# Optimization experiments

Measured on AMD Instinct MI355X. Metric: run time of the kernel, lower is better.

## Reference

```python
import jax, jax.numpy as jnp
import numpy as np

HIDDEN = 1024
HEADS = 16
HEAD_DIM = HIDDEN // HEADS


def setup_inputs() -> dict:
    key = jax.random.key(0)
    ks = jax.random.split(key, 8)
    B, S = 2, 2048
    scale = 1.0 / np.sqrt(HIDDEN)
    inp = {
        "hidden_states": jax.random.normal(ks[0], (B, S, HIDDEN), dtype=jnp.float32),
        "attention_mask": jnp.zeros((B, 1, 1, S), dtype=jnp.float32),
        "q_w": jax.random.normal(ks[1], (HIDDEN, HIDDEN), dtype=jnp.float32) * scale,
        "q_b": jnp.zeros((HIDDEN,), dtype=jnp.float32),
        "k_w": jax.random.normal(ks[2], (HIDDEN, HIDDEN), dtype=jnp.float32) * scale,
        "k_b": jnp.zeros((HIDDEN,), dtype=jnp.float32),
        "v_w": jax.random.normal(ks[3], (HIDDEN, HIDDEN), dtype=jnp.float32) * scale,
        "v_b": jnp.zeros((HIDDEN,), dtype=jnp.float32),
    }
    return inp


def _split_heads(x):
    # [B, S, H] -> [B, heads, S, head_dim]
    B, S, _ = x.shape
    return x.reshape(B, S, HEADS, HEAD_DIM).transpose(0, 2, 1, 3)


def reference(hidden_states, attention_mask, q_w, q_b, k_w, k_b, v_w, v_b):
    # Linear projections (torch Linear: x @ W.T + b; here weights stored as [in, out])
    q = _split_heads(hidden_states @ q_w + q_b)  # [B, h, S, d]
    k = _split_heads(hidden_states @ k_w + k_b)
    v = _split_heads(hidden_states @ v_w + v_b)

    scores = jnp.einsum("bhqd,bhkd->bhqk", q, k) / jnp.sqrt(jnp.float32(HEAD_DIM))
    scores = scores + attention_mask  # additive mask, broadcast [B,1,1,S]
    probs = jax.nn.softmax(scores, axis=-1)
    # dropout prob = 0.0 -> identity
    ctx = jnp.einsum("bhqk,bhkd->bhqd", probs, v)  # [B, h, S, d]
    B, _, S, _ = ctx.shape
    ctx = ctx.transpose(0, 2, 1, 3).reshape(B, S, HIDDEN)
    return ctx
```

## Files before the change

### kernel.cpp

```cpp
#include <hip/hip_runtime.h>

typedef __bf16 bf16;
typedef __attribute__((ext_vector_type(8))) __bf16 bf16x8;
typedef __attribute__((ext_vector_type(4))) __bf16 bf16x4;
typedef __attribute__((ext_vector_type(4))) float f32x4;
typedef __attribute__((ext_vector_type(2))) unsigned int uint2v;
typedef __attribute__((ext_vector_type(4))) unsigned int uint4v;

#define MFMA(a, b, c) __builtin_amdgcn_mfma_f32_16x16x32_bf16((a), (b), (c), 0, 0, 0)
#define LOG2E 1.44269504088896340736f

__device__ __forceinline__ bf16x8 cvt8(float4 a, float4 b) {
  bf16x8 r;
  r[0] = (bf16)a.x; r[1] = (bf16)a.y; r[2] = (bf16)a.z; r[3] = (bf16)a.w;
  r[4] = (bf16)b.x; r[5] = (bf16)b.y; r[6] = (bf16)b.z; r[7] = (bf16)b.w;
  return r;
}

__device__ __forceinline__ void stage16(const bf16* g, bf16* l) {
  __builtin_amdgcn_global_load_lds(
      (const __attribute__((address_space(1))) void*)g,
      (__attribute__((address_space(3))) void*)l, 16, 0, 0);
}

__global__ __launch_bounds__(256)
void cvt(const float* __restrict__ hs, const float* __restrict__ qw,
         const float* __restrict__ kw, const float* __restrict__ vw,
         bf16* __restrict__ Xb, bf16* __restrict__ Wt) {
  const int bid = blockIdx.x, tid = threadIdx.x;
  if (bid < 2048) {
    size_t off = (size_t)bid * 2048 + tid * 8;
    float4 x0 = *(const float4*)(hs + off);
    float4 x1 = *(const float4*)(hs + off + 4);
    *(bf16x8*)(Xb + off) = cvt8(x0, x1);
  } else {
    int t = bid - 2048;
    int z = t >> 8, ti = t & 255;
    const float* W = (z == 0) ? qw : (z == 1) ? kw : vw;
    int k0 = (ti >> 4) * 64, n0 = (ti & 15) * 64;
    __shared__ bf16 T[64 * 72];
    #pragma unroll
    for (int i = 0; i < 16; ++i) {
      int e = i * 256 + tid;
      int kr = e >> 6, nc = e & 63;
      T[nc * 72 + kr] = (bf16)W[(size_t)(k0 + kr) * 1024 + n0 + nc];
    }
    __syncthreads();
    #pragma unroll
    for (int i = 0; i < 2; ++i) {
      int e = i * 256 + tid;
      int nr = e >> 3, kg = e & 7;
      *(bf16x8*)(Wt + (size_t)z * 1048576 + (size_t)(n0 + nr) * 1024 + k0 + kg * 8) =
          *(const bf16x8*)&T[nr * 72 + kg * 8];
    }
  }
}

__global__ __launch_bounds__(256, 3)
void qkv_gemm(const bf16* __restrict__ Xb, const bf16* __restrict__ Wt,
              const float* __restrict__ qbias, const float* __restrict__ kbias,
              const float* __restrict__ vbias,
              bf16* __restrict__ qo, bf16* __restrict__ ko, bf16* __restrict__ vo) {
  const int blk = blockIdx.x;
  const int xcd = blk & 7, slot = blk >> 3;
  const int mb = xcd * 4 + slot / 24;
  const int nb = slot % 24;
  const int z = nb >> 3, nbm = nb & 7;
  const bf16* W = Wt + (size_t)z * 1048576;

  const int tid = threadIdx.x;
  const int wave = tid >> 6, lane = tid & 63, quad = lane >> 4, c = lane & 15;
  const int wr = wave >> 1, wc = wave & 1;
  const int lrow = lane >> 3;
  const int lg = (lane & 7) ^ lrow;

  __shared__ bf16 As[128 * 64];
  __shared__ bf16 Bs[128 * 64];

  f32x4 acc[4][4] = {};

  for (int k0 = 0; k0 < 1024; k0 += 64) {
    #pragma unroll
    for (int i = 0; i < 4; ++i) {
      int r = wave * 32 + i * 8;
      stage16(Xb + (size_t)(mb * 128 + r + lrow) * 1024 + k0 + lg * 8, &As[r * 64]);
      stage16(W + (size_t)(nbm * 128 + r + lrow) * 1024 + k0 + lg * 8, &Bs[r * 64]);
    }
    __syncthreads();
    #pragma unroll
    for (int ch = 0; ch < 2; ++ch) {
      bf16x8 af[4];
      #pragma unroll
      for (int rt = 0; rt < 4; ++rt) {
        int row = wr * 64 + rt * 16 + c;
        af[rt] = *(const bf16x8*)&As[row * 64 + ((((ch << 2) | quad) ^ (c & 7)) << 3)];
      }
      #pragma unroll
      for (int nt = 0; nt < 4; ++nt) {
        int row = wc * 64 + nt * 16 + c;
        bf16x8 bfrag = *(const bf16x8*)&Bs[row * 64 + ((((ch << 2) | quad) ^ (c & 7)) << 3)];
        #pragma unroll
        for (int rt = 0; rt < 4; ++rt)
          acc[rt][nt] = MFMA(af[rt], bfrag, acc[rt][nt]);
      }
    }
    __syncthreads();
  }

  const float* bias = (z == 0) ? qbias : (z == 1) ? kbias : vbias;
  float bv[4];
  #pragma unroll
  for (int nt = 0; nt < 4; ++nt)
    bv[nt] = bias[nbm * 128 + wc * 64 + nt * 16 + c];

  if (z == 2) {
    #pragma unroll
    for (int rt = 0; rt < 4; ++rt)
      #pragma unroll
      for (int nt = 0; nt < 4; ++nt) {
        int m0 = mb * 128 + wr * 64 + rt * 16 + 4 * quad;
        int n = nbm * 128 + wc * 64 + nt * 16 + c;
        bf16x4 pk;
        #pragma unroll
        for (int reg = 0; reg < 4; ++reg) pk[reg] = (bf16)(acc[rt][nt][reg] + bv[nt]);
        int b = m0 >> 11, s0 = m0 & 2047, h = n >> 6, d = n & 63;
        *(bf16x4*)&vo[(((size_t)b * 16 + h) * 64 + d) * 2048 + s0] = pk;
      }
  } else {
    bf16* dst = (z == 0) ? qo : ko;
    const float scale = (z == 0) ? 0.125f * LOG2E : 1.0f;
    #pragma unroll
    for (int rt = 0; rt < 4; ++rt)
      #pragma unroll
      for (int nt = 0; nt < 4; ++nt)
        #pragma unroll
        for (int reg = 0; reg < 4; ++reg) {
          float v = (acc[rt][nt][reg] + bv[nt]) * scale;
          int m = mb * 128 + wr * 64 + rt * 16 + 4 * quad + reg;
          int n = nbm * 128 + wc * 64 + nt * 16 + c;
          int b = m >> 11, s = m & 2047, h = n >> 6, d = n & 63;
          dst[(((size_t)b * 16 + h) * 2048 + s) * 64 + d] = (bf16)v;
        }
  }
}

__global__ __launch_bounds__(256, 4)
void attn(const bf16* __restrict__ qg, const bf16* __restrict__ kg,
          const bf16* __restrict__ vtg, const float* __restrict__ mask,
          float* __restrict__ out) {
  const int blk = blockIdx.x;
  const int xcd = blk & 7, slot = blk >> 3;
  const int bh = xcd * 4 + (slot >> 5);
  const int qblk = slot & 31;
  const int b = bh >> 4, h = bh & 15;
  const int tid = threadIdx.x;
  const int wave = tid >> 6, lane = tid & 63, quad = lane >> 4, c = lane & 15;
  const int lrow = lane >> 3, lg = (lane & 7) ^ lrow;

  __shared__ __align__(16) bf16 Ks[2][64 * 64];
  __shared__ __align__(16) bf16 Vs[2][64 * 64];
  __shared__ __align__(16) float Ms[2048];

  const bf16* qb_ = qg + (size_t)bh * 2048 * 64;
  const bf16* kb_ = kg + (size_t)bh * 2048 * 64;
  const bf16* vb_ = vtg + (size_t)bh * 64 * 2048;

  #pragma unroll
  for (int i = 0; i < 2; ++i) {
    int idx = i * 1024 + tid * 4;
    float4 m = *(const float4*)&mask[b * 2048 + idx];
    float4 ms = {m.x * LOG2E, m.y * LOG2E, m.z * LOG2E, m.w * LOG2E};
    *(float4*)&Ms[idx] = ms;
  }

  bf16x8 qf[2];
  #pragma unroll
  for (int ch = 0; ch < 2; ++ch)
    qf[ch] = *(const bf16x8*)(qb_ +
        (size_t)(qblk * 64 + wave * 16 + c) * 64 + ch * 32 + quad * 8);

  #pragma unroll
  for (int i = 0; i < 2; ++i) {
    int r = wave * 16 + i * 8;
    stage16(kb_ + (size_t)(r + lrow) * 64 + lg * 8, &Ks[0][r * 64]);
    stage16(vb_ + (size_t)(r + lrow) * 2048 + lg * 8, &Vs[0][r * 64]);
  }
  __asm__ volatile("s_waitcnt lgkmcnt(0)" ::: "memory");

  f32x4 o[4] = {};
  float lsum2[2] = {0.f, 0.f};

  for (int kt = 0; kt < 32; ++kt) {
    const int cur = kt & 1;
    __asm__ volatile("s_waitcnt vmcnt(0)" ::: "memory");
    __builtin_amdgcn_s_barrier();
    __builtin_amdgcn_sched_barrier(0);

    if (kt < 31) {
      #pragma unroll
      for (int i = 0; i < 2; ++i) {
        int r = wave * 16 + i * 8;
        stage16(kb_ + (size_t)((kt + 1) * 64 + r + lrow) * 64 + lg * 8,
                &Ks[cur ^ 1][r * 64]);
        stage16(vb_ + (size_t)(r + lrow) * 2048 + (kt + 1) * 64 + lg * 8,
                &Vs[cur ^ 1][r * 64]);
      }
    }
    __builtin_amdgcn_sched_barrier(0);

    f32x4 s[4];
    #pragma unroll
    for (int nt = 0; nt < 4; ++nt) {
      float4 mv = *(const float4*)&Ms[kt * 64 + nt * 16 + 4 * quad];
      f32x4 sv = {mv.x, mv.y, mv.z, mv.w};
      s[nt] = sv;
    }

    __builtin_amdgcn_s_setprio(1);
    #pragma unroll
    for (int nt = 0; nt < 4; ++nt)
      #pragma unroll
      for (int ch = 0; ch < 2; ++ch) {
        bf16x8 kf = *(const bf16x8*)&Ks[cur][(nt * 16 + c) * 64 +
                                            ((((ch << 2) | quad) ^ (c & 7)) << 3)];
        s[nt] = MFMA(kf, qf[ch], s[nt]);
      }
    __builtin_amdgcn_s_setprio(0);

    unsigned int U[4][2];
    #pragma unroll
    for (int nt = 0; nt < 4; ++nt) {
      bf16x4 pk;
      #pragma unroll
      for (int reg = 0; reg < 4; ++reg) {
        float p = __builtin_amdgcn_exp2f(s[nt][reg]);
        lsum2[nt & 1] += p;
        pk[reg] = (bf16)p;
      }
      uint2v uu = __builtin_bit_cast(uint2v, pk);
      U[nt][0] = uu.x; U[nt][1] = uu.y;
    }
    bf16x8 pa[2];
    #pragma unroll
    for (int ch = 0; ch < 2; ++ch) {
      unsigned int X0 = U[2 * ch][0],     X1 = U[2 * ch][1];
      unsigned int Y0 = U[2 * ch + 1][0], Y1 = U[2 * ch + 1][1];
      __asm__ volatile("v_permlane32_swap_b32 %0, %1" : "+v"(X0), "+v"(Y0));
      __asm__ volatile("v_permlane32_swap_b32 %0, %1" : "+v"(X1), "+v"(Y1));
      __asm__ volatile("v_permlane16_swap_b32 %0, %1" : "+v"(X0), "+v"(Y0));
      __asm__ volatile("v_permlane16_swap_b32 %0, %1" : "+v"(X1), "+v"(Y1));
      uint4v up = {X0, X1, Y0, Y1};
      pa[ch] = __builtin_bit_cast(bf16x8, up);
    }

    __builtin_amdgcn_s_setprio(1);
    #pragma unroll
    for (int ch = 0; ch < 2; ++ch)
      #pragma unroll
      for (int nt = 0; nt < 4; ++nt) {
        bf16x8 vf = *(const bf16x8*)&Vs[cur][(nt * 16 + c) * 64 +
                                            ((((ch << 2) | quad) ^ (c & 7)) << 3)];
        o[nt] = MFMA(vf, pa[ch], o[nt]);
      }
    __builtin_amdgcn_s_setprio(0);
  }

  {
    float l = lsum2[0] + lsum2[1];
    l += __shfl_xor(l, 16, 64);
    l += __shfl_xor(l, 32, 64);
    const float inv = 1.0f / l;
    const int srow = qblk * 64 + wave * 16 + c;
    #pragma unroll
    for (int nt = 0; nt < 4; ++nt) {
      float4 st = { o[nt][0] * inv, o[nt][1] * inv,
                    o[nt][2] * inv, o[nt][3] * inv };
      *(float4*)&out[((size_t)b * 2048 + srow) * 1024 + h * 64 + nt * 16 + 4 * quad] = st;
    }
  }
}

extern "C" void kernel_launch(void* const* d_in, const int* in_sizes, int n_in,
                              void* d_out, int out_size, void* d_ws, size_t ws_size,
                              hipStream_t stream) {
  const float* hs   = (const float*)d_in[0];
  const float* mask = (const float*)d_in[1];
  const float* qw   = (const float*)d_in[2];
  const float* qb   = (const float*)d_in[3];
  const float* kw   = (const float*)d_in[4];
  const float* kb   = (const float*)d_in[5];
  const float* vw   = (const float*)d_in[6];
  const float* vb   = (const float*)d_in[7];
  float* out = (float*)d_out;

  bf16* Xb   = (bf16*)d_ws;
  bf16* Wt   = Xb + (size_t)4096 * 1024;
  bf16* q_ws = Wt + (size_t)3 * 1048576;
  bf16* k_ws = q_ws + (size_t)4096 * 1024;
  bf16* v_ws = k_ws + (size_t)4096 * 1024;

  cvt<<<dim3(2816), 256, 0, stream>>>(hs, qw, kw, vw, Xb, Wt);
  qkv_gemm<<<dim3(768), 256, 0, stream>>>(Xb, Wt, qb, kb, vb, q_ws, k_ws, v_ws);
  attn<<<dim3(1024), 256, 0, stream>>>(q_ws, k_ws, v_ws, mask, out);
}
```

Measured before the change: 165.2 us.

## Split attention key tile across wave pairs with register-level Q reuse and LDS reduction

```diff
diff --git a/kernel.cpp b/kernel.cpp
--- a/kernel.cpp
+++ b/kernel.cpp
@@ -155,11 +155,12 @@
   const int b = bh >> 4, h = bh & 15;
   const int tid = threadIdx.x;
   const int wave = tid >> 6, lane = tid & 63, quad = lane >> 4, c = lane & 15;
+  const int w2 = wave & 1;
+  const int wq = wave >> 1;
   const int lrow = lane >> 3, lg = (lane & 7) ^ lrow;
 
-  __shared__ __align__(16) bf16 Ks[2][64 * 64];
-  __shared__ __align__(16) bf16 Vs[2][64 * 64];
-  __shared__ __align__(16) float Ms[2048];
+  __shared__ __align__(16) unsigned char SH[40960];
+  float* Ms = (float*)(SH + 32768);
 
   const bf16* qb_ = qg + (size_t)bh * 2048 * 64;
   const bf16* kb_ = kg + (size_t)bh * 2048 * 64;
@@ -173,110 +174,145 @@
     *(float4*)&Ms[idx] = ms;
   }
 
-  bf16x8 qf[2];
-  #pragma unroll
-  for (int ch = 0; ch < 2; ++ch)
-    qf[ch] = *(const bf16x8*)(qb_ +
-        (size_t)(qblk * 64 + wave * 16 + c) * 64 + ch * 32 + quad * 8);
+  bf16x8 qf[2][2];
+  #pragma unroll
+  for (int g = 0; g < 2; ++g)
+    #pragma unroll
+    for (int ch = 0; ch < 2; ++ch)
+      qf[g][ch] = *(const bf16x8*)(qb_ +
+          (size_t)(qblk * 64 + wq * 32 + g * 16 + c) * 64 + ch * 32 + quad * 8);
 
   #pragma unroll
   for (int i = 0; i < 2; ++i) {
     int r = wave * 16 + i * 8;
-    stage16(kb_ + (size_t)(r + lrow) * 64 + lg * 8, &Ks[0][r * 64]);
-    stage16(vb_ + (size_t)(r + lrow) * 2048 + lg * 8, &Vs[0][r * 64]);
+    stage16(kb_ + (size_t)(r + lrow) * 64 + lg * 8, (bf16*)SH + r * 64);
+    stage16(vb_ + (size_t)(r + lrow) * 2048 + lg * 8, (bf16*)(SH + 16384) + r * 64);
   }
   __asm__ volatile("s_waitcnt lgkmcnt(0)" ::: "memory");
 
-  f32x4 o[4] = {};
-  float lsum2[2] = {0.f, 0.f};
+  f32x4 o[4][2] = {};
+  float lsum[2] = {0.f, 0.f};
 
   for (int kt = 0; kt < 32; ++kt) {
     const int cur = kt & 1;
+    bf16* Kc = (bf16*)(SH + cur * 8192);
+    bf16* Vc = (bf16*)(SH + 16384 + cur * 8192);
     __asm__ volatile("s_waitcnt vmcnt(0)" ::: "memory");
     __builtin_amdgcn_s_barrier();
     __builtin_amdgcn_sched_barrier(0);
 
     if (kt < 31) {
+      bf16* Kn = (bf16*)(SH + (cur ^ 1) * 8192);
+      bf16* Vn = (bf16*)(SH + 16384 + (cur ^ 1) * 8192);
       #pragma unroll
       for (int i = 0; i < 2; ++i) {
         int r = wave * 16 + i * 8;
-        stage16(kb_ + (size_t)((kt + 1) * 64 + r + lrow) * 64 + lg * 8,
-                &Ks[cur ^ 1][r * 64]);
-        stage16(vb_ + (size_t)(r + lrow) * 2048 + (kt + 1) * 64 + lg * 8,
-                &Vs[cur ^ 1][r * 64]);
+        stage16(kb_ + (size_t)((kt + 1) * 64 + r + lrow) * 64 + lg * 8, Kn + r * 64);
+        stage16(vb_ + (size_t)(r + lrow) * 2048 + (kt + 1) * 64 + lg * 8, Vn + r * 64);
       }
     }
     __builtin_amdgcn_sched_barrier(0);
 
-    f32x4 s[4];
-    #pragma unroll
-    for (int nt = 0; nt < 4; ++nt) {
-      float4 mv = *(const float4*)&Ms[kt * 64 + nt * 16 + 4 * quad];
+    f32x4 s[2][2];
+    #pragma unroll
+    for (int kt2 = 0; kt2 < 2; ++kt2) {
+      float4 mv = *(const float4*)&Ms[kt * 64 + w2 * 32 + kt2 * 16 + 4 * quad];
       f32x4 sv = {mv.x, mv.y, mv.z, mv.w};
-      s[nt] = sv;
+      s[0][kt2] = sv;
+      s[1][kt2] = sv;
     }
 
     __builtin_amdgcn_s_setprio(1);
     #pragma unroll
-    for (int nt = 0; nt < 4; ++nt)
+    for (int kt2 = 0; kt2 < 2; ++kt2)
       #pragma unroll
       for (int ch = 0; ch < 2; ++ch) {
-        bf16x8 kf = *(const bf16x8*)&Ks[cur][(nt * 16 + c) * 64 +
-                                            ((((ch << 2) | quad) ^ (c & 7)) << 3)];
-        s[nt] = MFMA(kf, qf[ch], s[nt]);
+        bf16x8 kf = *(const bf16x8*)&Kc[(w2 * 32 + kt2 * 16 + c) * 64 +
+                                        ((((ch << 2) | quad) ^ (c & 7)) << 3)];
+        s[0][kt2] = MFMA(kf, qf[0][ch], s[0][kt2]);
+        s[1][kt2] = MFMA(kf, qf[1][ch], s[1][kt2]);
       }
     __builtin_amdgcn_s_setprio(0);
 
-    unsigned int U[4][2];
-    #pragma unroll
-    for (int nt = 0; nt < 4; ++nt) {
-      bf16x4 pk;
-      #pragma unroll
-      for (int reg = 0; reg < 4; ++reg) {
-        float p = __builtin_amdgcn_exp2f(s[nt][reg]);
-        lsum2[nt & 1] += p;
-        pk[reg] = (bf16)p;
-      }
-      uint2v uu = __builtin_bit_cast(uint2v, pk);
-      U[nt][0] = uu.x; U[nt][1] = uu.y;
-    }
-    bf16x8 pa[2];
-    #pragma unroll
-    for (int ch = 0; ch < 2; ++ch) {
-      unsigned int X0 = U[2 * ch][0],     X1 = U[2 * ch][1];
-      unsigned int Y0 = U[2 * ch + 1][0], Y1 = U[2 * ch + 1][1];
-      __asm__ volatile("v_permlane32_swap_b32 %0, %1" : "+v"(X0), "+v"(Y0));
-      __asm__ volatile("v_permlane32_swap_b32 %0, %1" : "+v"(X1), "+v"(Y1));
-      __asm__ volatile("v_permlane16_swap_b32 %0, %1" : "+v"(X0), "+v"(Y0));
-      __asm__ volatile("v_permlane16_swap_b32 %0, %1" : "+v"(X1), "+v"(Y1));
-      uint4v up = {X0, X1, Y0, Y1};
-      pa[ch] = __builtin_bit_cast(bf16x8, up);
+    bf16x8 pf[2];
+    #pragma unroll
+    for (int g = 0; g < 2; ++g) {
+      unsigned int A0, A1, B0, B1;
+      {
+        bf16x4 pk;
+        #pragma unroll
+        for (int reg = 0; reg < 4; ++reg) {
+          float p = __builtin_amdgcn_exp2f(s[g][0][reg]);
+          lsum[g] += p;
+          pk[reg] = (bf16)p;
+        }
+        uint2v uu = __builtin_bit_cast(uint2v, pk);
+        A0 = uu.x; A1 = uu.y;
+      }
+      {
+        bf16x4 pk;
+        #pragma unroll
+        for (int reg = 0; reg < 4; ++reg) {
+          float p = __builtin_amdgcn_exp2f(s[g][1][reg]);
+          lsum[g] += p;
+          pk[reg] = (bf16)p;
+        }
+        uint2v uu = __builtin_bit_cast(uint2v, pk);
+        B0 = uu.x; B1 = uu.y;
+      }
+      __asm__ volatile("v_permlane32_swap_b32 %0, %1" : "+v"(A0), "+v"(B0));
+      __asm__ volatile("v_permlane32_swap_b32 %0, %1" : "+v"(A1), "+v"(B1));
+      __asm__ volatile("v_permlane16_swap_b32 %0, %1" : "+v"(A0), "+v"(B0));
+      __asm__ volatile("v_permlane16_swap_b32 %0, %1" : "+v"(A1), "+v"(B1));
+      uint4v up = {A0, A1, B0, B1};
+      pf[g] = __builtin_bit_cast(bf16x8, up);
     }
 
     __builtin_amdgcn_s_setprio(1);
     #pragma unroll
-    for (int ch = 0; ch < 2; ++ch)
-      #pragma unroll
-      for (int nt = 0; nt < 4; ++nt) {
-        bf16x8 vf = *(const bf16x8*)&Vs[cur][(nt * 16 + c) * 64 +
-                                            ((((ch << 2) | quad) ^ (c & 7)) << 3)];
-        o[nt] = MFMA(vf, pa[ch], o[nt]);
-      }
+    for (int dt = 0; dt < 4; ++dt) {
+      bf16x8 vf = *(const bf16x8*)&Vc[(dt * 16 + c) * 64 +
+                                      ((((w2 << 2) | quad) ^ (c & 7)) << 3)];
+      o[dt][0] = MFMA(vf, pf[0], o[dt][0]);
+      o[dt][1] = MFMA(vf, pf[1], o[dt][1]);
+    }
     __builtin_amdgcn_s_setprio(0);
   }
 
-  {
-    float l = lsum2[0] + lsum2[1];
-    l += __shfl_xor(l, 16, 64);
-    l += __shfl_xor(l, 32, 64);
-    const float inv = 1.0f / l;
-    const int srow = qblk * 64 + wave * 16 + c;
-    #pragma unroll
-    for (int nt = 0; nt < 4; ++nt) {
-      float4 st = { o[nt][0] * inv, o[nt][1] * inv,
-                    o[nt][2] * inv, o[nt][3] * inv };
-      *(float4*)&out[((size_t)b * 2048 + srow) * 1024 + h * 64 + nt * 16 + 4 * quad] = st;
-    }
+  #pragma unroll
+  for (int g = 0; g < 2; ++g) {
+    lsum[g] += __shfl_xor(lsum[g], 16, 64);
+    lsum[g] += __shfl_xor(lsum[g], 32, 64);
+  }
+
+  __syncthreads();
+  float* rec = (float*)(SH + (size_t)(wq * 64 + lane) * 144);
+  if (w2 == 1) {
+    #pragma unroll
+    for (int dt = 0; dt < 4; ++dt)
+      #pragma unroll
+      for (int g = 0; g < 2; ++g)
+        *(f32x4*)&rec[(dt * 2 + g) * 4] = o[dt][g];
+    rec[32] = lsum[0];
+    rec[33] = lsum[1];
+  }
+  __syncthreads();
+  if (w2 == 0) {
+    float inv[2];
+    #pragma unroll
+    for (int g = 0; g < 2; ++g) inv[g] = 1.0f / (lsum[g] + rec[32 + g]);
+    #pragma unroll
+    for (int dt = 0; dt < 4; ++dt)
+      #pragma unroll
+      for (int g = 0; g < 2; ++g) {
+        f32x4 po = *(const f32x4*)&rec[(dt * 2 + g) * 4];
+        const int srow = qblk * 64 + wq * 32 + g * 16 + c;
+        float4 st = { (o[dt][g][0] + po[0]) * inv[g],
+                      (o[dt][g][1] + po[1]) * inv[g],
+                      (o[dt][g][2] + po[2]) * inv[g],
+                      (o[dt][g][3] + po[3]) * inv[g] };
+        *(float4*)&out[((size_t)b * 2048 + srow) * 1024 + h * 64 + dt * 16 + 4 * quad] = st;
+      }
   }
 }
 
```

Result: faster. 161.3 us (median of 3 runs) (-2.3%).
